# Performance work log

Hardware: AMD Instinct MI355X
Metric: run time of the kernel (lower is better)

The kernel has to match this reference:

```python
import jax, jax.numpy as jnp
import numpy as np
import math

# ---- surrogate ternary spike (forward only needs the primal) ----
def surrogate_spike(m):
    return jnp.clip(jnp.round(m), -1.0, 1.0)

def rmsnorm(x, gamma):
    # torch: F.normalize(x, dim=-1) * dim**0.5 * (gamma + 1)
    n = jnp.linalg.norm(x, axis=-1, keepdims=True)
    return x / jnp.maximum(n, 1e-12) * (x.shape[-1] ** 0.5) * (gamma + 1.0)

DIM = 1024
HEADS = 8
HEAD_DIM = DIM // HEADS          # 128
INNER = int(HEAD_DIM * 1.5)      # 192
FF_INNER = int(DIM * 4 * 2 / 3)  # 2730
B, L = 8, 2048
BETA0 = 0.9

def setup_inputs() -> dict:
    key = jax.random.key(0)
    ks = jax.random.split(key, 10)
    s = 0.02
    beta_raw0 = math.log(BETA0 / (1.0 - BETA0))
    return {
        "x": jax.random.normal(ks[0], (B, L, DIM), dtype=jnp.float32),
        "in_gamma": jnp.zeros((DIM,), jnp.float32),
        "gate_W": jax.random.normal(ks[1], (HEADS, INNER, HEAD_DIM), jnp.float32) * s,
        "cand_W": jax.random.normal(ks[2], (HEADS, INNER, HEAD_DIM), jnp.float32) * s,
        "out_W": jax.random.normal(ks[3], (HEADS, HEAD_DIM, INNER), jnp.float32) * s,
        "gate_beta_raw": jnp.full((HEADS, INNER), beta_raw0, jnp.float32),
        "gate_theta": jnp.ones((HEADS, INNER), jnp.float32),
        "cand_beta_raw": jnp.full((HEADS, INNER), beta_raw0, jnp.float32),
        "cand_theta": jnp.ones((HEADS, INNER), jnp.float32),
        "ff_gamma": jnp.zeros((DIM,), jnp.float32),
        "ffg_W": jax.random.normal(ks[4], (FF_INNER, DIM), jnp.float32) * s,
        "ffu_W": jax.random.normal(ks[5], (FF_INNER, DIM), jnp.float32) * s,
        "ffd_W": jax.random.normal(ks[6], (DIM, FF_INNER), jnp.float32) * s,
    }

def reference(x, in_gamma, gate_W, cand_W, out_W, gate_beta_raw, gate_theta,
              cand_beta_raw, cand_theta, ff_gamma, ffg_W, ffu_W, ffd_W):
    Bv, Lv, Dv = x.shape
    res_scale = 1.0 / math.sqrt(1.0)  # num_layers = 1

    xn = rmsnorm(x, in_gamma)                      # [B,L,D]
    xh = xn.reshape(Bv, Lv, HEADS, HEAD_DIM)       # split heads along dim
    xh = jnp.transpose(xh, (1, 0, 2, 3))           # [L,B,H,hd] for scan

    beta_g = jax.nn.sigmoid(gate_beta_raw)         # [H,inner]
    beta_c = jax.nn.sigmoid(cand_beta_raw)

    h0 = jnp.zeros((Bv, HEADS, INNER), x.dtype)
    gm0 = jnp.zeros_like(h0)
    cm0 = jnp.zeros_like(h0)

    def step(carry, xt):
        h, gm, cm = carry
        # gate branch: SI-LIF(Linear(x))
        gc = jnp.einsum('bhd,hid->bhi', xt, gate_W)
        gm = beta_g * gm + gc
        gs = surrogate_spike(gm)
        gm = gm - gs * gate_theta
        z = (gs + 1.0) * 0.5
        # candidate branch
        cc = jnp.einsum('bhd,hid->bhi', xt, cand_W)
        cm = beta_c * cm + cc
        cs = surrogate_spike(cm)
        cm = cm - cs * cand_theta
        # minGRU lerp update + output projection
        h = (1.0 - z) * h + z * cs
        out = jnp.einsum('bhi,hdi->bhd', h, out_W)  # [B,H,hd]
        return (h, gm, cm), out

    _, outs = jax.lax.scan(step, (h0, gm0, cm0), xh)   # outs [L,B,H,hd]
    gru_out = jnp.transpose(outs, (1, 0, 2, 3)).reshape(Bv, Lv, Dv)

    x = x + res_scale * gru_out                    # dropout is identity at eval
    fn = rmsnorm(x, ff_gamma)
    ff = jnp.einsum('blf,df->bld',
                    jax.nn.silu(jnp.einsum('bld,fd->blf', fn, ffg_W))
                    * jnp.einsum('bld,fd->blf', fn, ffu_W),
                    ffd_W)
    x = x + res_scale * ff
    return x
```

## Files before the change

### kernel.cpp

```cpp
#include <hip/hip_runtime.h>
#include <stdint.h>

#define NDIM   1024
#define NHEADS 8
#define NHD    128
#define NINNER 192
#define NFF    2730
#define NFFP   2816
#define NB     8
#define NL     2048
#define NBL    16384
#define NSTATE (NB * NHEADS * NINNER)

typedef short  short8 __attribute__((ext_vector_type(8)));
typedef float  f32x4  __attribute__((ext_vector_type(4)));

__device__ __forceinline__ unsigned short f2bf(float f) {
  union { float f; uint32_t u; } v; v.f = f;
  uint32_t r = (v.u + 0x7FFFu + ((v.u >> 16) & 1u)) >> 16;
  return (unsigned short)r;
}

__device__ __forceinline__ void gload16(const void* g, void* l) {
  __builtin_amdgcn_global_load_lds(
      (const __attribute__((address_space(1))) uint32_t*)g,
      (__attribute__((address_space(3))) uint32_t*)l, 16, 0, 0);
}

__device__ __forceinline__ f32x4 mfma_bf16(short8 a, short8 b, f32x4 c) {
  return __builtin_amdgcn_mfma_f32_16x16x32_bf16(a, b, c, 0, 0, 0);
}

__global__ __launch_bounds__(256) void rscale_kernel(
    const float* __restrict__ xin, float* __restrict__ rscale) {
  int row = blockIdx.x, t = threadIdx.x;
  float4 v = ((const float4*)(xin + (size_t)row * NDIM))[t];
  float ss = v.x * v.x + v.y * v.y + v.z * v.z + v.w * v.w;
  #pragma unroll
  for (int off = 32; off > 0; off >>= 1) ss += __shfl_xor(ss, off, 64);
  __shared__ float wss[4];
  if ((t & 63) == 0) wss[t >> 6] = ss;
  __syncthreads();
  if (t == 0) {
    ss = wss[0] + wss[1] + wss[2] + wss[3];
    rscale[row] = 32.0f / fmaxf(sqrtf(ss), 1e-12f);
  }
}

__global__ __launch_bounds__(256) void rms_bf16_kernel(
    const float* __restrict__ xin, const float* __restrict__ gamma,
    unsigned short* __restrict__ outb) {
  int row = blockIdx.x, t = threadIdx.x;
  float4 v = ((const float4*)(xin + (size_t)row * NDIM))[t];
  float ss = v.x * v.x + v.y * v.y + v.z * v.z + v.w * v.w;
  #pragma unroll
  for (int off = 32; off > 0; off >>= 1) ss += __shfl_xor(ss, off, 64);
  __shared__ float wss[4];
  if ((t & 63) == 0) wss[t >> 6] = ss;
  __syncthreads();
  ss = wss[0] + wss[1] + wss[2] + wss[3];
  float scale = 32.0f / fmaxf(sqrtf(ss), 1e-12f);
  float4 gv = ((const float4*)gamma)[t];
  ushort4 ob;
  ob.x = f2bf(v.x * scale * (1.0f + gv.x));
  ob.y = f2bf(v.y * scale * (1.0f + gv.y));
  ob.z = f2bf(v.z * scale * (1.0f + gv.z));
  ob.w = f2bf(v.w * scale * (1.0f + gv.w));
  ((ushort4*)outb)[(size_t)row * 256 + t] = ob;
}

__global__ __launch_bounds__(256) void inproj_kernel(
    const float* __restrict__ x, const float* __restrict__ rscale,
    const float* __restrict__ gamma, const float* __restrict__ gate_W,
    const float* __restrict__ cand_W, float* __restrict__ gcb,
    float* __restrict__ ccb, int l_base, int LCL) {
  __shared__ float lA[64 * NHD];
  __shared__ float lW[64 * NHD];
  int mt = blockIdx.x, h = blockIdx.y, z = blockIdx.z;
  int branch = z / 3, nt = z % 3, n0 = nt * 64;
  const float* W = (branch == 0 ? gate_W : cand_W)
                 + (size_t)h * NINNER * NHD + (size_t)n0 * NHD;
  float* outp = (branch == 0 ? gcb : ccb);
  int t = threadIdx.x;
  #pragma unroll
  for (int i = 0; i < 8; i++) {
    int c = t + i * 256;
    int r = c >> 5, c4 = c & 31;
    int m = mt * 64 + r, ll = m >> 3, b = m & 7;
    int xrow = b * NL + l_base + ll;
    float4 xv = *(const float4*)(x + (size_t)xrow * NDIM + h * NHD + c4 * 4);
    float rs = rscale[xrow];
    float4 gv = *(const float4*)(gamma + h * NHD + c4 * 4);
    float4 o;
    o.x = xv.x * rs * (1.0f + gv.x);
    o.y = xv.y * rs * (1.0f + gv.y);
    o.z = xv.z * rs * (1.0f + gv.z);
    o.w = xv.w * rs * (1.0f + gv.w);
    *(float4*)&lA[r * NHD + c4 * 4] = o;
    *(float4*)&lW[r * NHD + (((c4 ^ (r & 7)) & 31) * 4)] =
        *(const float4*)(W + (size_t)r * NHD + c4 * 4);
  }
  __syncthreads();
  int tr = t >> 4, tc = t & 15;
  int swz = (tc & 7) << 2;
  float acc[4][4] = {};
  #pragma unroll 4
  for (int k4 = 0; k4 < 32; k4++) {
    float4 a[4];
    #pragma unroll
    for (int m = 0; m < 4; m++) a[m] = *(float4*)&lA[(tr * 4 + m) * NHD + k4 * 4];
    #pragma unroll
    for (int j = 0; j < 4; j++) {
      int rowb = (tc + 16 * j) * NHD;
      float w0 = lW[rowb + ((k4 * 4 + 0) ^ swz)];
      float w1 = lW[rowb + ((k4 * 4 + 1) ^ swz)];
      float w2 = lW[rowb + ((k4 * 4 + 2) ^ swz)];
      float w3 = lW[rowb + ((k4 * 4 + 3) ^ swz)];
      #pragma unroll
      for (int m = 0; m < 4; m++) {
        acc[m][j] = fmaf(a[m].x, w0, acc[m][j]);
        acc[m][j] = fmaf(a[m].y, w1, acc[m][j]);
        acc[m][j] = fmaf(a[m].z, w2, acc[m][j]);
        acc[m][j] = fmaf(a[m].w, w3, acc[m][j]);
      }
    }
  }
  #pragma unroll
  for (int m = 0; m < 4; m++) {
    int mm = mt * 64 + tr * 4 + m;
    int ll = mm >> 3, b = mm & 7;
    size_t rowo = ((size_t)((h * NB + b) << LCL) + ll) * NINNER + n0 + tc;
    #pragma unroll
    for (int j = 0; j < 4; j++) outp[rowo + 16 * j] = acc[m][j];
  }
}

__global__ __launch_bounds__(192) void scan_kernel(
    const float* __restrict__ gcb, const float* __restrict__ ccb,
    const float* __restrict__ gbr, const float* __restrict__ gth,
    const float* __restrict__ cbr, const float* __restrict__ cth,
    unsigned short* __restrict__ hbuf, float* __restrict__ state,
    int first, int CL, int LCL) {
  int b = blockIdx.x >> 3, h = blockIdx.x & 7;
  int i = threadIdx.x;
  int pi = h * NINNER + i;
  float beta_g = 1.0f / (1.0f + expf(-gbr[pi]));
  float beta_c = 1.0f / (1.0f + expf(-cbr[pi]));
  float thg = gth[pi], thc = cth[pi];
  size_t sbase = ((size_t)(b * NHEADS + h)) * NINNER + i;
  size_t pbase = ((size_t)((h * NB + b) << LCL)) * NINNER + i;
  const float* pg = gcb + pbase;
  const float* pc = ccb + pbase;
  unsigned short* ph = hbuf + pbase;
  float gm, cm, hs;
  if (first) { gm = 0.f; cm = 0.f; hs = 0.f; }
  else { gm = state[sbase]; cm = state[NSTATE + sbase]; hs = state[2 * NSTATE + sbase]; }
  const int CH = 16;
  float gq[CH], cq[CH];
  #pragma unroll
  for (int u = 0; u < CH; u++) { gq[u] = pg[u * NINNER]; cq[u] = pc[u * NINNER]; }
  int NIT = CL / CH;
  for (int ch = 0; ch < NIT; ch++) {
    float gn[CH], cn[CH];
    bool more = (ch + 1) < NIT;
    if (more) {
      size_t nb = (size_t)(ch + 1) * CH * NINNER;
      #pragma unroll
      for (int u = 0; u < CH; u++) { gn[u] = pg[nb + u * NINNER]; cn[u] = pc[nb + u * NINNER]; }
    }
    #pragma unroll
    for (int u = 0; u < CH; u++) {
      gm = fmaf(beta_g, gm, gq[u]);
      float gs = fminf(fmaxf(rintf(gm), -1.f), 1.f);
      gm -= gs * thg;
      float z = (gs + 1.f) * 0.5f;
      cm = fmaf(beta_c, cm, cq[u]);
      float cs = fminf(fmaxf(rintf(cm), -1.f), 1.f);
      cm -= cs * thc;
      hs = (1.f - z) * hs + z * cs;
      ph[((size_t)(ch * CH + u)) * NINNER] = f2bf(hs);
    }
    if (more) {
      #pragma unroll
      for (int u = 0; u < CH; u++) { gq[u] = gn[u]; cq[u] = cn[u]; }
    }
  }
  state[sbase] = gm; state[NSTATE + sbase] = cm; state[2 * NSTATE + sbase] = hs;
}

__global__ __launch_bounds__(256) void outproj_kernel(
    const unsigned short* __restrict__ hbuf, const unsigned short* __restrict__ wob,
    const float* __restrict__ x, float* __restrict__ x2, int l_base, int LCL) {
  __shared__ short lA[128 * 32], lB[128 * 32];
  int t = threadIdx.x, lane = t & 63, wave = t >> 6;
  int wr = wave >> 1, wc = wave & 1;
  int m0 = blockIdx.x * 128;
  int h = blockIdx.y;
  const unsigned short* Ab = hbuf + ((size_t)(h * NB) << LCL) * NINNER;
  const unsigned short* Bb = wob + (size_t)h * NHD * NINNER;
  f32x4 z4 = {0.f, 0.f, 0.f, 0.f};
  f32x4 acc[4][4];
  #pragma unroll
  for (int i = 0; i < 4; i++)
    #pragma unroll
    for (int j = 0; j < 4; j++) acc[i][j] = z4;
  int rl = lane & 15, kq = (lane >> 4) * 8;
  for (int ks = 0; ks < NINNER / 32; ks++) {
    int k0 = ks * 32;
    #pragma unroll
    for (int it = 0; it < 2; it++) {
      int c = t + it * 256;
      int r = c >> 2, c8 = (c & 3) * 8;
      gload16(Ab + (size_t)(m0 + r) * NINNER + k0 + c8, &lA[c * 8]);
      gload16(Bb + (size_t)r * NINNER + k0 + c8, &lB[c * 8]);
    }
    __syncthreads();
    short8 a[4], bb[4];
    #pragma unroll
    for (int mi = 0; mi < 4; mi++)
      a[mi] = *(const short8*)&lA[(wr * 64 + mi * 16 + rl) * 32 + kq];
    #pragma unroll
    for (int ni = 0; ni < 4; ni++)
      bb[ni] = *(const short8*)&lB[(wc * 64 + ni * 16 + rl) * 32 + kq];
    #pragma unroll
    for (int mi = 0; mi < 4; mi++)
      #pragma unroll
      for (int ni = 0; ni < 4; ni++)
        acc[mi][ni] = mfma_bf16(a[mi], bb[ni], acc[mi][ni]);
    __syncthreads();
  }
  int CLm1 = (1 << LCL) - 1;
  #pragma unroll
  for (int mi = 0; mi < 4; mi++)
    #pragma unroll
    for (int ni = 0; ni < 4; ni++) {
      int rowl = m0 + wr * 64 + mi * 16 + (lane >> 4) * 4;
      int col = wc * 64 + ni * 16 + rl;
      #pragma unroll
      for (int r = 0; r < 4; r++) {
        int rr = rowl + r;
        int b = rr >> LCL, ll = rr & CLm1;
        size_t off = ((size_t)(b * NL + l_base + ll)) * NDIM + h * NHD + col;
        x2[off] = x[off] + acc[mi][ni][r];
      }
    }
}

__global__ __launch_bounds__(256) void pack_gu_kernel(
    const float* __restrict__ ffg, const float* __restrict__ ffu,
    unsigned short* __restrict__ wg, unsigned short* __restrict__ wu) {
  int row = blockIdx.x, t = threadIdx.x;
  const float* src = (blockIdx.y == 0) ? ffg : ffu;
  unsigned short* dst = (blockIdx.y == 0) ? wg : wu;
  ushort4 o;
  if (row < NFF) {
    float4 v = *(const float4*)(src + (size_t)row * NDIM + t * 4);
    o.x = f2bf(v.x); o.y = f2bf(v.y); o.z = f2bf(v.z); o.w = f2bf(v.w);
  } else { o.x = 0; o.y = 0; o.z = 0; o.w = 0; }
  *(ushort4*)(dst + (size_t)row * NDIM + t * 4) = o;
}

__global__ __launch_bounds__(256) void pack_d_kernel(
    const float* __restrict__ ffd, unsigned short* __restrict__ wd) {
  int row = blockIdx.x;
  for (int c = threadIdx.x; c < NFFP; c += 256) {
    float v = (c < NFF) ? ffd[(size_t)row * NFF + c] : 0.0f;
    wd[(size_t)row * NFFP + c] = f2bf(v);
  }
}

__global__ __launch_bounds__(256) void pack_flat_kernel(
    const float* __restrict__ src, unsigned short* __restrict__ dst, int n) {
  int i = blockIdx.x * 256 + threadIdx.x;
  if (i < n) dst[i] = f2bf(src[i]);
}

__global__ __launch_bounds__(256) void gateup_kernel(
    const unsigned short* __restrict__ fnb, const unsigned short* __restrict__ wg,
    const unsigned short* __restrict__ wu, unsigned short* __restrict__ act,
    int m_base, int nwg) {
  __shared__ short lA[128 * 32], lG[64 * 32], lU[64 * 32];
  int q = nwg >> 3;
  int hw = blockIdx.x;
  int work = (hw & 7) * q + (hw >> 3);
  int mt = work / 44, ntl = work % 44;
  int t = threadIdx.x, lane = t & 63, wave = t >> 6;
  int wr = wave >> 1, wc = wave & 1;
  int m0l = mt * 128;
  int m0g = m_base + m0l;
  int n0 = ntl * 64;
  f32x4 z4 = {0.f, 0.f, 0.f, 0.f};
  f32x4 accg[4][2], accu[4][2];
  #pragma unroll
  for (int i = 0; i < 4; i++)
    #pragma unroll
    for (int j = 0; j < 2; j++) { accg[i][j] = z4; accu[i][j] = z4; }
  int rl = lane & 15, kq = (lane >> 4) * 8;
  for (int ks = 0; ks < NDIM / 32; ks++) {
    int k0 = ks * 32;
    {
      #pragma unroll
      for (int it = 0; it < 2; it++) {
        int c = t + it * 256;
        int r = c >> 2, c8 = (c & 3) * 8;
        gload16(fnb + (size_t)(m0g + r) * NDIM + k0 + c8, &lA[c * 8]);
      }
      int r = t >> 2, c8 = (t & 3) * 8;
      gload16(wg + (size_t)(n0 + r) * NDIM + k0 + c8, &lG[t * 8]);
      gload16(wu + (size_t)(n0 + r) * NDIM + k0 + c8, &lU[t * 8]);
    }
    __syncthreads();
    short8 a[4], bg[2], bu[2];
    #pragma unroll
    for (int mi = 0; mi < 4; mi++)
      a[mi] = *(const short8*)&lA[(wr * 64 + mi * 16 + rl) * 32 + kq];
    #pragma unroll
    for (int ni = 0; ni < 2; ni++) {
      bg[ni] = *(const short8*)&lG[(wc * 32 + ni * 16 + rl) * 32 + kq];
      bu[ni] = *(const short8*)&lU[(wc * 32 + ni * 16 + rl) * 32 + kq];
    }
    #pragma unroll
    for (int mi = 0; mi < 4; mi++)
      #pragma unroll
      for (int ni = 0; ni < 2; ni++) {
        accg[mi][ni] = mfma_bf16(a[mi], bg[ni], accg[mi][ni]);
        accu[mi][ni] = mfma_bf16(a[mi], bu[ni], accu[mi][ni]);
      }
    __syncthreads();
  }
  #pragma unroll
  for (int mi = 0; mi < 4; mi++)
    #pragma unroll
    for (int ni = 0; ni < 2; ni++) {
      int rowl = m0l + wr * 64 + mi * 16 + (lane >> 4) * 4;
      int col = n0 + wc * 32 + ni * 16 + rl;
      #pragma unroll
      for (int r = 0; r < 4; r++) {
        float g = accg[mi][ni][r], u = accu[mi][ni][r];
        float s = g / (1.0f + expf(-g)) * u;
        act[(size_t)(rowl + r) * NFFP + col] = f2bf(s);
      }
    }
}

__global__ __launch_bounds__(256) void down_kernel(
    const unsigned short* __restrict__ act, const unsigned short* __restrict__ wd,
    const float* resid, float* outp, int m_base, int nwg) {
  __shared__ short lA[128 * 32], lB[128 * 32];
  int q = nwg >> 3;
  int hw = blockIdx.x;
  int work = (hw & 7) * q + (hw >> 3);
  int mt = work >> 3, ntl = work & 7;
  int t = threadIdx.x, lane = t & 63, wave = t >> 6;
  int wr = wave >> 1, wc = wave & 1;
  int m0l = mt * 128;
  int n0 = ntl * 128;
  f32x4 z4 = {0.f, 0.f, 0.f, 0.f};
  f32x4 acc[4][4];
  #pragma unroll
  for (int i = 0; i < 4; i++)
    #pragma unroll
    for (int j = 0; j < 4; j++) acc[i][j] = z4;
  int rl = lane & 15, kq = (lane >> 4) * 8;
  for (int ks = 0; ks < NFFP / 32; ks++) {
    int k0 = ks * 32;
    #pragma unroll
    for (int it = 0; it < 2; it++) {
      int c = t + it * 256;
      int r = c >> 2, c8 = (c & 3) * 8;
      gload16(act + (size_t)(m0l + r) * NFFP + k0 + c8, &lA[c * 8]);
      gload16(wd  + (size_t)(n0 + r) * NFFP + k0 + c8, &lB[c * 8]);
    }
    __syncthreads();
    short8 a[4], bb[4];
    #pragma unroll
    for (int mi = 0; mi < 4; mi++)
      a[mi] = *(const short8*)&lA[(wr * 64 + mi * 16 + rl) * 32 + kq];
    #pragma unroll
    for (int ni = 0; ni < 4; ni++)
      bb[ni] = *(const short8*)&lB[(wc * 64 + ni * 16 + rl) * 32 + kq];
    #pragma unroll
    for (int mi = 0; mi < 4; mi++)
      #pragma unroll
      for (int ni = 0; ni < 4; ni++)
        acc[mi][ni] = mfma_bf16(a[mi], bb[ni], acc[mi][ni]);
    __syncthreads();
  }
  #pragma unroll
  for (int mi = 0; mi < 4; mi++)
    #pragma unroll
    for (int ni = 0; ni < 4; ni++) {
      int rowg = m_base + m0l + wr * 64 + mi * 16 + (lane >> 4) * 4;
      int col = n0 + wc * 64 + ni * 16 + rl;
      #pragma unroll
      for (int r = 0; r < 4; r++) {
        size_t off = (size_t)(rowg + r) * NDIM + col;
        outp[off] = resid[off] + acc[mi][ni][r];
      }
    }
}

extern "C" void kernel_launch(void* const* d_in, const int* in_sizes, int n_in,
                              void* d_out, int out_size, void* d_ws, size_t ws_size,
                              hipStream_t stream) {
  const float* x        = (const float*)d_in[0];
  const float* in_gamma = (const float*)d_in[1];
  const float* gate_W   = (const float*)d_in[2];
  const float* cand_W   = (const float*)d_in[3];
  const float* out_W    = (const float*)d_in[4];
  const float* gbr      = (const float*)d_in[5];
  const float* gth      = (const float*)d_in[6];
  const float* cbr      = (const float*)d_in[7];
  const float* cth      = (const float*)d_in[8];
  const float* ff_gamma = (const float*)d_in[9];
  const float* ffg      = (const float*)d_in[10];
  const float* ffu      = (const float*)d_in[11];
  const float* ffd      = (const float*)d_in[12];
  float* outp = (float*)d_out;

  char* p = (char*)d_ws;
  float* rscale = (float*)p;              p += 65536;
  float* state  = (float*)p;              p += 3 * NSTATE * 4;
  unsigned short* wgb = (unsigned short*)p; p += (size_t)NFFP * NDIM * 2;
  unsigned short* wub = (unsigned short*)p; p += (size_t)NFFP * NDIM * 2;
  unsigned short* wdb = (unsigned short*)p; p += (size_t)NDIM * NFFP * 2;
  unsigned short* wob = (unsigned short*)p; p += (size_t)NHEADS * NHD * NINNER * 2;
  unsigned short* fnb = (unsigned short*)p; p += (size_t)NBL * NDIM * 2;
  char* region = p;
  size_t fixed = (size_t)(region - (char*)d_ws);
  size_t avail = ws_size > fixed ? ws_size - fixed : 0;

  int CL = NL;
  while (CL > 128 && (size_t)CL * 122880ULL > avail) CL >>= 1;
  int MC = NBL;
  while (MC > 1024 && (size_t)MC * 5632ULL > avail) MC >>= 1;
  int LCL = 0; while ((1 << LCL) < CL) LCL++;

  float* gcb = (float*)region;
  float* ccb = (float*)(region + (size_t)CL * NSTATE * 4);
  unsigned short* hbuf = (unsigned short*)(region + (size_t)CL * NSTATE * 8);
  unsigned short* act  = (unsigned short*)region;

  pack_gu_kernel<<<dim3(NFFP, 2), 256, 0, stream>>>(ffg, ffu, wgb, wub);
  pack_d_kernel<<<NDIM, 256, 0, stream>>>(ffd, wdb);
  pack_flat_kernel<<<(NHEADS * NHD * NINNER + 255) / 256, 256, 0, stream>>>(
      out_W, wob, NHEADS * NHD * NINNER);
  rscale_kernel<<<NBL, 256, 0, stream>>>(x, rscale);

  int NCH = NL / CL;
  for (int c = 0; c < NCH; c++) {
    inproj_kernel<<<dim3(CL / 8, 8, 6), 256, 0, stream>>>(
        x, rscale, in_gamma, gate_W, cand_W, gcb, ccb, c * CL, LCL);
    scan_kernel<<<64, 192, 0, stream>>>(
        gcb, ccb, gbr, gth, cbr, cth, hbuf, state, (c == 0) ? 1 : 0, CL, LCL);
    outproj_kernel<<<dim3(NB * CL / 128, NHEADS), 256, 0, stream>>>(
        hbuf, wob, x, outp, c * CL, LCL);
  }

  rms_bf16_kernel<<<NBL, 256, 0, stream>>>(outp, ff_gamma, fnb);

  int NMC = NBL / MC;
  for (int mc = 0; mc < NMC; mc++) {
    int nwg_gu = (MC / 128) * 44;
    int nwg_dn = (MC / 128) * 8;
    gateup_kernel<<<nwg_gu, 256, 0, stream>>>(fnb, wgb, wub, act, mc * MC, nwg_gu);
    down_kernel<<<nwg_dn, 256, 0, stream>>>(act, wdb, outp, outp, mc * MC, nwg_dn);
  }
}
```

Baseline: 1.050 ms.

## Spread scan across more blocks, deepen prefetch, and double GEMM K-tile to 64

```diff
diff --git a/kernel.cpp b/kernel.cpp
--- a/kernel.cpp
+++ b/kernel.cpp
@@ -135,14 +135,15 @@
   }
 }
 
-__global__ __launch_bounds__(192) void scan_kernel(
+__global__ __launch_bounds__(64) void scan_kernel(
     const float* __restrict__ gcb, const float* __restrict__ ccb,
     const float* __restrict__ gbr, const float* __restrict__ gth,
     const float* __restrict__ cbr, const float* __restrict__ cth,
     unsigned short* __restrict__ hbuf, float* __restrict__ state,
     int first, int CL, int LCL) {
-  int b = blockIdx.x >> 3, h = blockIdx.x & 7;
-  int i = threadIdx.x;
+  int bh = blockIdx.x / 3, third = blockIdx.x % 3;
+  int b = bh >> 3, h = bh & 7;
+  int i = third * 64 + threadIdx.x;
   int pi = h * NINNER + i;
   float beta_g = 1.0f / (1.0f + expf(-gbr[pi]));
   float beta_c = 1.0f / (1.0f + expf(-cbr[pi]));
@@ -155,7 +156,7 @@
   float gm, cm, hs;
   if (first) { gm = 0.f; cm = 0.f; hs = 0.f; }
   else { gm = state[sbase]; cm = state[NSTATE + sbase]; hs = state[2 * NSTATE + sbase]; }
-  const int CH = 16;
+  const int CH = 32;
   float gq[CH], cq[CH];
   #pragma unroll
   for (int u = 0; u < CH; u++) { gq[u] = pg[u * NINNER]; cq[u] = pc[u * NINNER]; }
@@ -279,7 +280,7 @@
     const unsigned short* __restrict__ fnb, const unsigned short* __restrict__ wg,
     const unsigned short* __restrict__ wu, unsigned short* __restrict__ act,
     int m_base, int nwg) {
-  __shared__ short lA[128 * 32], lG[64 * 32], lU[64 * 32];
+  __shared__ short lA[128 * 64], lG[64 * 64], lU[64 * 64];
   int q = nwg >> 3;
   int hw = blockIdx.x;
   int work = (hw & 7) * q + (hw >> 3);
@@ -296,36 +297,42 @@
     #pragma unroll
     for (int j = 0; j < 2; j++) { accg[i][j] = z4; accu[i][j] = z4; }
   int rl = lane & 15, kq = (lane >> 4) * 8;
-  for (int ks = 0; ks < NDIM / 32; ks++) {
-    int k0 = ks * 32;
-    {
-      #pragma unroll
-      for (int it = 0; it < 2; it++) {
-        int c = t + it * 256;
-        int r = c >> 2, c8 = (c & 3) * 8;
-        gload16(fnb + (size_t)(m0g + r) * NDIM + k0 + c8, &lA[c * 8]);
+  for (int ks = 0; ks < NDIM / 64; ks++) {
+    int k0 = ks * 64;
+    #pragma unroll
+    for (int it = 0; it < 4; it++) {
+      int c = t + it * 256;
+      int r = c >> 3, c8 = (c & 7) * 8;
+      gload16(fnb + (size_t)(m0g + r) * NDIM + k0 + c8, &lA[c * 8]);
+    }
+    #pragma unroll
+    for (int it = 0; it < 2; it++) {
+      int c = t + it * 256;
+      int r = c >> 3, c8 = (c & 7) * 8;
+      gload16(wg + (size_t)(n0 + r) * NDIM + k0 + c8, &lG[c * 8]);
+      gload16(wu + (size_t)(n0 + r) * NDIM + k0 + c8, &lU[c * 8]);
+    }
+    __syncthreads();
+    #pragma unroll
+    for (int kh = 0; kh < 2; kh++) {
+      int ko = kh * 32 + kq;
+      short8 a[4], bg[2], bu[2];
+      #pragma unroll
+      for (int mi = 0; mi < 4; mi++)
+        a[mi] = *(const short8*)&lA[(wr * 64 + mi * 16 + rl) * 64 + ko];
+      #pragma unroll
+      for (int ni = 0; ni < 2; ni++) {
+        bg[ni] = *(const short8*)&lG[(wc * 32 + ni * 16 + rl) * 64 + ko];
+        bu[ni] = *(const short8*)&lU[(wc * 32 + ni * 16 + rl) * 64 + ko];
       }
-      int r = t >> 2, c8 = (t & 3) * 8;
-      gload16(wg + (size_t)(n0 + r) * NDIM + k0 + c8, &lG[t * 8]);
-      gload16(wu + (size_t)(n0 + r) * NDIM + k0 + c8, &lU[t * 8]);
-    }
-    __syncthreads();
-    short8 a[4], bg[2], bu[2];
-    #pragma unroll
-    for (int mi = 0; mi < 4; mi++)
-      a[mi] = *(const short8*)&lA[(wr * 64 + mi * 16 + rl) * 32 + kq];
-    #pragma unroll
-    for (int ni = 0; ni < 2; ni++) {
-      bg[ni] = *(const short8*)&lG[(wc * 32 + ni * 16 + rl) * 32 + kq];
-      bu[ni] = *(const short8*)&lU[(wc * 32 + ni * 16 + rl) * 32 + kq];
-    }
-    #pragma unroll
-    for (int mi = 0; mi < 4; mi++)
-      #pragma unroll
-      for (int ni = 0; ni < 2; ni++) {
-        accg[mi][ni] = mfma_bf16(a[mi], bg[ni], accg[mi][ni]);
-        accu[mi][ni] = mfma_bf16(a[mi], bu[ni], accu[mi][ni]);
-      }
+      #pragma unroll
+      for (int mi = 0; mi < 4; mi++)
+        #pragma unroll
+        for (int ni = 0; ni < 2; ni++) {
+          accg[mi][ni] = mfma_bf16(a[mi], bg[ni], accg[mi][ni]);
+          accu[mi][ni] = mfma_bf16(a[mi], bu[ni], accu[mi][ni]);
+        }
+    }
     __syncthreads();
   }
   #pragma unroll
@@ -346,7 +353,7 @@
 __global__ __launch_bounds__(256) void down_kernel(
     const unsigned short* __restrict__ act, const unsigned short* __restrict__ wd,
     const float* resid, float* outp, int m_base, int nwg) {
-  __shared__ short lA[128 * 32], lB[128 * 32];
+  __shared__ short lA[128 * 64], lB[128 * 64];
   int q = nwg >> 3;
   int hw = blockIdx.x;
   int work = (hw & 7) * q + (hw >> 3);
@@ -362,28 +369,32 @@
     #pragma unroll
     for (int j = 0; j < 4; j++) acc[i][j] = z4;
   int rl = lane & 15, kq = (lane >> 4) * 8;
-  for (int ks = 0; ks < NFFP / 32; ks++) {
-    int k0 = ks * 32;
-    #pragma unroll
-    for (int it = 0; it < 2; it++) {
+  for (int ks = 0; ks < NFFP / 64; ks++) {
+    int k0 = ks * 64;
+    #pragma unroll
+    for (int it = 0; it < 4; it++) {
       int c = t + it * 256;
-      int r = c >> 2, c8 = (c & 3) * 8;
+      int r = c >> 3, c8 = (c & 7) * 8;
       gload16(act + (size_t)(m0l + r) * NFFP + k0 + c8, &lA[c * 8]);
       gload16(wd  + (size_t)(n0 + r) * NFFP + k0 + c8, &lB[c * 8]);
     }
     __syncthreads();
-    short8 a[4], bb[4];
-    #pragma unroll
-    for (int mi = 0; mi < 4; mi++)
-      a[mi] = *(const short8*)&lA[(wr * 64 + mi * 16 + rl) * 32 + kq];
-    #pragma unroll
-    for (int ni = 0; ni < 4; ni++)
-      bb[ni] = *(const short8*)&lB[(wc * 64 + ni * 16 + rl) * 32 + kq];
-    #pragma unroll
-    for (int mi = 0; mi < 4; mi++)
+    #pragma unroll
+    for (int kh = 0; kh < 2; kh++) {
+      int ko = kh * 32 + kq;
+      short8 a[4], bb[4];
+      #pragma unroll
+      for (int mi = 0; mi < 4; mi++)
+        a[mi] = *(const short8*)&lA[(wr * 64 + mi * 16 + rl) * 64 + ko];
       #pragma unroll
       for (int ni = 0; ni < 4; ni++)
-        acc[mi][ni] = mfma_bf16(a[mi], bb[ni], acc[mi][ni]);
+        bb[ni] = *(const short8*)&lB[(wc * 64 + ni * 16 + rl) * 64 + ko];
+      #pragma unroll
+      for (int mi = 0; mi < 4; mi++)
+        #pragma unroll
+        for (int ni = 0; ni < 4; ni++)
+          acc[mi][ni] = mfma_bf16(a[mi], bb[ni], acc[mi][ni]);
+    }
     __syncthreads();
   }
   #pragma unroll
@@ -451,7 +462,7 @@
   for (int c = 0; c < NCH; c++) {
     inproj_kernel<<<dim3(CL / 8, 8, 6), 256, 0, stream>>>(
         x, rscale, in_gamma, gate_W, cand_W, gcb, ccb, c * CL, LCL);
-    scan_kernel<<<64, 192, 0, stream>>>(
+    scan_kernel<<<192, 64, 0, stream>>>(
         gcb, ccb, gbr, gth, cbr, cth, hbuf, state, (c == 0) ? 1 : 0, CL, LCL);
     outproj_kernel<<<dim3(NB * CL / 128, NHEADS), 256, 0, stream>>>(
         hbuf, wob, x, outp, c * CL, LCL);
```

New measurement: 1.115 ms. +6.2%, slower.

## Vectorize inproj LDS reads and split scan into more single-wave blocks

Applied to the files above, without the earlier changes.

```diff
diff --git a/kernel.cpp b/kernel.cpp
--- a/kernel.cpp
+++ b/kernel.cpp
@@ -96,34 +96,34 @@
     o.y = xv.y * rs * (1.0f + gv.y);
     o.z = xv.z * rs * (1.0f + gv.z);
     o.w = xv.w * rs * (1.0f + gv.w);
-    *(float4*)&lA[r * NHD + c4 * 4] = o;
-    *(float4*)&lW[r * NHD + (((c4 ^ (r & 7)) & 31) * 4)] =
+    *(float4*)&lA[r * NHD + ((c4 ^ (r & 7)) * 4)] = o;
+    *(float4*)&lW[r * NHD + ((c4 ^ (r & 7)) * 4)] =
         *(const float4*)(W + (size_t)r * NHD + c4 * 4);
   }
   __syncthreads();
   int tr = t >> 4, tc = t & 15;
-  int swz = (tc & 7) << 2;
+  int wkey = tc & 7;
   float acc[4][4] = {};
   #pragma unroll 4
   for (int k4 = 0; k4 < 32; k4++) {
-    float4 a[4];
-    #pragma unroll
-    for (int m = 0; m < 4; m++) a[m] = *(float4*)&lA[(tr * 4 + m) * NHD + k4 * 4];
-    #pragma unroll
-    for (int j = 0; j < 4; j++) {
-      int rowb = (tc + 16 * j) * NHD;
-      float w0 = lW[rowb + ((k4 * 4 + 0) ^ swz)];
-      float w1 = lW[rowb + ((k4 * 4 + 1) ^ swz)];
-      float w2 = lW[rowb + ((k4 * 4 + 2) ^ swz)];
-      float w3 = lW[rowb + ((k4 * 4 + 3) ^ swz)];
-      #pragma unroll
-      for (int m = 0; m < 4; m++) {
-        acc[m][j] = fmaf(a[m].x, w0, acc[m][j]);
-        acc[m][j] = fmaf(a[m].y, w1, acc[m][j]);
-        acc[m][j] = fmaf(a[m].z, w2, acc[m][j]);
-        acc[m][j] = fmaf(a[m].w, w3, acc[m][j]);
-      }
-    }
+    float4 a[4], w[4];
+    #pragma unroll
+    for (int m = 0; m < 4; m++) {
+      int row = tr * 4 + m;
+      a[m] = *(float4*)&lA[row * NHD + ((k4 ^ (row & 7)) * 4)];
+    }
+    #pragma unroll
+    for (int j = 0; j < 4; j++)
+      w[j] = *(const float4*)&lW[(tc + 16 * j) * NHD + ((k4 ^ wkey) * 4)];
+    #pragma unroll
+    for (int m = 0; m < 4; m++)
+      #pragma unroll
+      for (int j = 0; j < 4; j++) {
+        acc[m][j] = fmaf(a[m].x, w[j].x, acc[m][j]);
+        acc[m][j] = fmaf(a[m].y, w[j].y, acc[m][j]);
+        acc[m][j] = fmaf(a[m].z, w[j].z, acc[m][j]);
+        acc[m][j] = fmaf(a[m].w, w[j].w, acc[m][j]);
+      }
   }
   #pragma unroll
   for (int m = 0; m < 4; m++) {
@@ -135,14 +135,15 @@
   }
 }
 
-__global__ __launch_bounds__(192) void scan_kernel(
+__global__ __launch_bounds__(64) void scan_kernel(
     const float* __restrict__ gcb, const float* __restrict__ ccb,
     const float* __restrict__ gbr, const float* __restrict__ gth,
     const float* __restrict__ cbr, const float* __restrict__ cth,
     unsigned short* __restrict__ hbuf, float* __restrict__ state,
     int first, int CL, int LCL) {
-  int b = blockIdx.x >> 3, h = blockIdx.x & 7;
-  int i = threadIdx.x;
+  int bh = blockIdx.x / 3, third = blockIdx.x % 3;
+  int b = bh >> 3, h = bh & 7;
+  int i = third * 64 + threadIdx.x;
   int pi = h * NINNER + i;
   float beta_g = 1.0f / (1.0f + expf(-gbr[pi]));
   float beta_c = 1.0f / (1.0f + expf(-cbr[pi]));
@@ -155,7 +156,7 @@
   float gm, cm, hs;
   if (first) { gm = 0.f; cm = 0.f; hs = 0.f; }
   else { gm = state[sbase]; cm = state[NSTATE + sbase]; hs = state[2 * NSTATE + sbase]; }
-  const int CH = 16;
+  const int CH = 32;
   float gq[CH], cq[CH];
   #pragma unroll
   for (int u = 0; u < CH; u++) { gq[u] = pg[u * NINNER]; cq[u] = pc[u * NINNER]; }
@@ -451,7 +452,7 @@
   for (int c = 0; c < NCH; c++) {
     inproj_kernel<<<dim3(CL / 8, 8, 6), 256, 0, stream>>>(
         x, rscale, in_gamma, gate_W, cand_W, gcb, ccb, c * CL, LCL);
-    scan_kernel<<<64, 192, 0, stream>>>(
+    scan_kernel<<<192, 64, 0, stream>>>(
         gcb, ccb, gbr, gth, cbr, cth, hbuf, state, (c == 0) ? 1 : 0, CL, LCL);
     outproj_kernel<<<dim3(NB * CL / 128, NHEADS), 256, 0, stream>>>(
         hbuf, wob, x, outp, c * CL, LCL);
```

After: 943.9 us. 10.1% less time.
